# Kernel optimization log

Hardware: AMD Instinct MI355X
Metric: run time of the kernel (lower is better)

Reference implementation:

```python
import jax, jax.numpy as jnp
import numpy as np


def _unpack_int4(w_i32):
    # w_i32: [N, K//8] int32, 8 signed int4 nibbles per int32 (low nibble first)
    shifts = jnp.arange(8, dtype=jnp.int32) * 4
    nib = (w_i32[:, :, None] >> shifts[None, None, :]) & 0xF  # [N, K//8, 8]
    signed = (nib ^ 8) - 8  # map [0,15] -> [-8,7]
    N = w_i32.shape[0]
    return signed.reshape(N, -1)  # [N, K] int32 in [-8,7]


def setup_inputs() -> dict:
    key = jax.random.key(0)
    k1, k2, k3, k4, k5 = jax.random.split(key, 5)
    M, K, N, G = 4096, 4096, 14336, 128
    qx = jax.random.normal(k1, (M, K), dtype=jnp.float32)
    qxscale = jax.random.uniform(k2, (M, 1), dtype=jnp.float32, minval=0.5, maxval=1.5)
    weight_i4 = jax.random.randint(k3, (N, K // 8), 0, 2147483647, dtype=jnp.int32)
    weight_scale = jax.random.uniform(k4, (N, K // G), dtype=jnp.float32, minval=0.001, maxval=0.02)
    bias = jax.random.normal(k5, (N,), dtype=jnp.float32) * 0.02
    return {"qx": qx, "qxscale": qxscale, "weight_i4": weight_i4,
            "weight_scale": weight_scale, "bias": bias, "group_size": G}


def reference(qx, qxscale, weight_i4, weight_scale, bias, group_size):
    # 1) unpack int32 -> int4  2) per-group dequant  3) matmul  4) scale+bias  5) silu
    iweight = _unpack_int4(weight_i4)  # [N, K]
    N, K = iweight.shape
    deq_w = (iweight.astype(jnp.float32).reshape(N, K // group_size, group_size)
             * weight_scale[:, :, None]).reshape(N, K)  # [N, K]
    y = jnp.einsum('mk,nk->mn', qx, deq_w) * qxscale  # [M, N]
    y = y + bias[None, :]
    return jax.nn.silu(y)
```

## Files before the change

### kernel.cpp

```cpp
#include <hip/hip_runtime.h>
#include <hip/hip_bf16.h>
#include <stdint.h>


#define M_DIM 4096
#define K_DIM 4096
#define N_DIM 14336
#define GSZ   128

typedef __bf16 bf16x8 __attribute__((ext_vector_type(8)));
typedef __bf16 bf16x4 __attribute__((ext_vector_type(4)));
typedef float  f32x4  __attribute__((ext_vector_type(4)));

#define GLOAD16(g, l) __builtin_amdgcn_global_load_lds( \
    (const __attribute__((address_space(1))) void*)(g), \
    (__attribute__((address_space(3))) void*)(l), 16, 0, 0)

#define WAITVM(N) asm volatile("s_waitcnt vmcnt(" #N ")" ::: "memory")


__global__ __launch_bounds__(256) void convertA_kernel(
    const float* __restrict__ qx, __bf16* __restrict__ out)
{
    const size_t i = ((size_t)blockIdx.x * 256 + threadIdx.x) * 8;
    const float4 a = *(const float4*)(qx + i);
    const float4 b = *(const float4*)(qx + i + 4);
    bf16x8 v;
    v[0] = (__bf16)a.x; v[1] = (__bf16)a.y; v[2] = (__bf16)a.z; v[3] = (__bf16)a.w;
    v[4] = (__bf16)b.x; v[5] = (__bf16)b.y; v[6] = (__bf16)b.z; v[7] = (__bf16)b.w;
    *(bf16x8*)(out + i) = v;
}

__global__ __launch_bounds__(256) void dequantW_kernel(
    const int* __restrict__ wq, const float* __restrict__ wscale,
    __bf16* __restrict__ out)
{
    const size_t g = (size_t)blockIdx.x * 256 + threadIdx.x;
    const int n  = (int)(g >> 9);
    const int wi = (int)(g & 511);
    const float s = wscale[(size_t)n * (K_DIM / GSZ) + (wi >> 4)];
    const int w = wq[g];
    bf16x8 v;
    #pragma unroll
    for (int j = 0; j < 8; ++j) {
        const int q = ((int)((unsigned)w << (28 - 4 * j))) >> 28;
        v[j] = (__bf16)((float)q * s);
    }
    *(bf16x8*)(out + g * 8) = v;
}


constexpr int BM = 256, BN = 256, BK = 32;
constexpr int NT = K_DIM / BK;
constexpr int BUF_BYTES = 32768;

__global__ __launch_bounds__(512, 2) void gemm256_kernel(
    const __bf16* __restrict__ A,
    const __bf16* __restrict__ B,
    const float* __restrict__ qxscale,
    const float* __restrict__ bias,
    float* __restrict__ out)
{
    __shared__ __align__(16) char smem[4 * BUF_BYTES];

    const int t    = threadIdx.x;
    const int lane = t & 63;
    const int wave = t >> 6;
    const int wr   = wave >> 2;
    const int wc   = wave & 3;

    const int bid = blockIdx.x;
    const int cpx = (M_DIM / BM) * (N_DIM / BN) / 8;
    const int wg  = (bid & 7) * cpx + (bid >> 3);
    const int tiles_n = N_DIM / BN;
    const int tm = wg / tiles_n, tn = wg % tiles_n;
    const int m0 = tm * BM, n0 = tn * BN;

    const int srow = t >> 2;
    const int scb  = ((t & 3) * 16) ^ (((t >> 3) & 3) << 4);
    const char* aS = (const char*)A + (size_t)(m0 + srow) * K_DIM * 2 + scb;
    const char* bS = (const char*)B + (size_t)(n0 + srow) * K_DIM * 2 + scb;
    const size_t sweepG = (size_t)128 * K_DIM * 2;
    char* sbase = smem;

    auto STAGE_A = [&](int kt) {
        char* d = sbase + (kt & 3) * BUF_BYTES + t * 16;
        const char* s = aS + (size_t)kt * 64;
        GLOAD16(s, d);
        GLOAD16(s + sweepG, d + 8192);
    };
    auto STAGE_B = [&](int kt) {
        char* d = sbase + (kt & 3) * BUF_BYTES + 16384 + t * 16;
        const char* s = bS + (size_t)kt * 64;
        GLOAD16(s, d);
        GLOAD16(s + sweepG, d + 8192);
    };

    const int lane15 = lane & 15;
    const int pkb = ((lane >> 4) * 16) ^ (((lane >> 1) & 3) << 4);
    const int aRowB = (wr * 128 + lane15) * 64 + pkb;
    const int bRowB = (wc * 64 + lane15) * 64 + pkb + 16384;

    f32x4 acc[8][4] = {};

    STAGE_A(0); STAGE_B(0);
    STAGE_A(1); STAGE_B(1);
    STAGE_A(2); STAGE_B(2);
    WAITVM(8);
    __builtin_amdgcn_s_barrier();
    __builtin_amdgcn_sched_barrier(0);

    for (int kt = 0; kt < NT; ++kt) {
        const char* buf = sbase + (kt & 3) * BUF_BYTES;
        bf16x8 af[8], bf[4];

        #pragma unroll
        for (int ni = 0; ni < 4; ++ni)
            bf[ni] = *(const bf16x8*)(buf + bRowB + ni * 1024);
        #pragma unroll
        for (int mi = 0; mi < 8; ++mi)
            af[mi] = *(const bf16x8*)(buf + aRowB + mi * 1024);

        if (kt + 3 < NT) { STAGE_A(kt + 3); STAGE_B(kt + 3); }

        __builtin_amdgcn_s_setprio(1);
        #pragma unroll
        for (int mi = 0; mi < 8; ++mi)
            #pragma unroll
            for (int ni = 0; ni < 4; ++ni)
                acc[mi][ni] = __builtin_amdgcn_mfma_f32_16x16x32_bf16(
                    af[mi], bf[ni], acc[mi][ni], 0, 0, 0);
        __builtin_amdgcn_s_setprio(0);

        if (kt + 1 < NT) {
            if (kt + 3 < NT)      WAITVM(8);
            else if (kt + 2 < NT) WAITVM(4);
            else                  WAITVM(0);
            __builtin_amdgcn_s_barrier();
            __builtin_amdgcn_sched_barrier(0);
        }
    }

    const int c_col = lane & 15;
    const int c_r4  = (lane >> 4) * 4;
    #pragma unroll
    for (int mi = 0; mi < 8; ++mi) {
        const int mg = m0 + wr * 128 + mi * 16 + c_r4;
        float qs[4];
        #pragma unroll
        for (int r = 0; r < 4; ++r) qs[r] = qxscale[mg + r];
        #pragma unroll
        for (int ni = 0; ni < 4; ++ni) {
            const int ng = n0 + wc * 64 + ni * 16 + c_col;
            const float bv = bias[ng];
            #pragma unroll
            for (int r = 0; r < 4; ++r) {
                const float y = acc[mi][ni][r] * qs[r] + bv;
                out[(size_t)(mg + r) * N_DIM + ng] = y / (1.f + __expf(-y));
            }
        }
    }
}


constexpr int FBM = 128, FBN = 128, FBK = 64;
constexpr int FLDA = 72;

__global__ __launch_bounds__(256) void gateproj_fused_kernel(
    const float* __restrict__ qx, const float* __restrict__ qxscale,
    const int* __restrict__ wq, const float* __restrict__ wscale,
    const float* __restrict__ bias, float* __restrict__ out)
{
    __shared__ __bf16 sA[FBM * FLDA];
    __shared__ __bf16 sB[FBN * FLDA];

    const int tid  = threadIdx.x;
    const int lane = tid & 63;
    const int wave = tid >> 6;
    const int wm = wave >> 1, wn = wave & 1;

    const int bid = blockIdx.x;
    const int cpx = (M_DIM / FBM) * (N_DIM / FBN) / 8;
    const int wg  = (bid & 7) * cpx + (bid >> 3);
    const int tiles_n = N_DIM / FBN;
    const int tm = wg / tiles_n, tn = wg % tiles_n;
    const int m0 = tm * FBM, n0 = tn * FBN;

    const int a_row = tid >> 4;
    const int a_col = (tid & 15) * 4;
    const float* aPtr = qx + (size_t)(m0 + a_row) * K_DIM + a_col;

    const int b_row = tid >> 1;
    const int b_wb  = (tid & 1) * 4;
    const int*   bPtr = wq     + (size_t)(n0 + b_row) * (K_DIM / 8) + b_wb;
    const float* sPtr = wscale + (size_t)(n0 + b_row) * (K_DIM / GSZ);

    float4 aReg[8];
    int    bRegW[4];
    float  bScl;
    f32x4 acc[4][4] = {};

    auto LOAD = [&](int kt) {
        const float* ap = aPtr + kt * FBK;
        #pragma unroll
        for (int i = 0; i < 8; ++i)
            aReg[i] = *(const float4*)(ap + (size_t)i * 16 * K_DIM);
        int4 b = *(const int4*)(bPtr + kt * 8);
        bRegW[0] = b.x; bRegW[1] = b.y; bRegW[2] = b.z; bRegW[3] = b.w;
        bScl = sPtr[kt >> 1];
    };

    auto STORE = [&]() {
        #pragma unroll
        for (int i = 0; i < 8; ++i) {
            bf16x4 v;
            v[0] = (__bf16)aReg[i].x; v[1] = (__bf16)aReg[i].y;
            v[2] = (__bf16)aReg[i].z; v[3] = (__bf16)aReg[i].w;
            *(bf16x4*)&sA[(a_row + i * 16) * FLDA + a_col] = v;
        }
        const int cb = (tid & 1) * 32;
        #pragma unroll
        for (int wi = 0; wi < 4; ++wi) {
            const int w = bRegW[wi];
            bf16x8 o;
            #pragma unroll
            for (int j = 0; j < 8; ++j) {
                const int v = ((int)((unsigned)w << (28 - 4 * j))) >> 28;
                o[j] = (__bf16)((float)v * bScl);
            }
            *(bf16x8*)&sB[b_row * FLDA + cb + wi * 8] = o;
        }
    };

    LOAD(0); STORE(); __syncthreads();

    const int FNT = K_DIM / FBK;
    for (int kt = 0; kt < FNT; ++kt) {
        if (kt + 1 < FNT) LOAD(kt + 1);
        #pragma unroll
        for (int kk = 0; kk < 2; ++kk) {
            bf16x8 af[4], bfr[4];
            const int ko = kk * 32 + (lane >> 4) * 8;
            #pragma unroll
            for (int mi = 0; mi < 4; ++mi)
                af[mi] = *(const bf16x8*)&sA[(wm * 64 + mi * 16 + (lane & 15)) * FLDA + ko];
            #pragma unroll
            for (int ni = 0; ni < 4; ++ni)
                bfr[ni] = *(const bf16x8*)&sB[(wn * 64 + ni * 16 + (lane & 15)) * FLDA + ko];
            #pragma unroll
            for (int mi = 0; mi < 4; ++mi)
                #pragma unroll
                for (int ni = 0; ni < 4; ++ni)
                    acc[mi][ni] = __builtin_amdgcn_mfma_f32_16x16x32_bf16(
                        af[mi], bfr[ni], acc[mi][ni], 0, 0, 0);
        }
        __syncthreads();
        if (kt + 1 < FNT) { STORE(); __syncthreads(); }
    }

    const int c_col = lane & 15;
    const int c_r4  = (lane >> 4) * 4;
    #pragma unroll
    for (int mi = 0; mi < 4; ++mi) {
        const int mg = m0 + wm * 64 + mi * 16 + c_r4;
        float qs[4];
        #pragma unroll
        for (int r = 0; r < 4; ++r) qs[r] = qxscale[mg + r];
        #pragma unroll
        for (int ni = 0; ni < 4; ++ni) {
            const int ng = n0 + wn * 64 + ni * 16 + c_col;
            const float bv = bias[ng];
            #pragma unroll
            for (int r = 0; r < 4; ++r) {
                const float y = acc[mi][ni][r] * qs[r] + bv;
                out[(size_t)(mg + r) * N_DIM + ng] = y / (1.f + __expf(-y));
            }
        }
    }
}


extern "C" void kernel_launch(void* const* d_in, const int* in_sizes, int n_in,
                              void* d_out, int out_size, void* d_ws, size_t ws_size,
                              hipStream_t stream) {
    const float* qx      = (const float*)d_in[0];
    const float* qxscale = (const float*)d_in[1];
    const int*   wq      = (const int*)d_in[2];
    const float* wscale  = (const float*)d_in[3];
    const float* bias    = (const float*)d_in[4];
    float* out = (float*)d_out;

    const size_t needA = (size_t)M_DIM * K_DIM * 2;
    const size_t needW = (size_t)N_DIM * K_DIM * 2;

    if (ws_size >= needA + needW) {
        __bf16* Abf = (__bf16*)d_ws;
        __bf16* Wbf = Abf + (size_t)M_DIM * K_DIM;

        hipLaunchKernelGGL(convertA_kernel, dim3(M_DIM * K_DIM / 8 / 256), dim3(256),
                           0, stream, qx, Abf);
        hipLaunchKernelGGL(dequantW_kernel, dim3(N_DIM * (K_DIM / 8) / 256), dim3(256),
                           0, stream, wq, wscale, Wbf);

        const int grid = (M_DIM / BM) * (N_DIM / BN);
        hipLaunchKernelGGL(gemm256_kernel, dim3(grid), dim3(512), 0, stream,
                           Abf, Wbf, qxscale, bias, out);
    } else {
        const int grid = (M_DIM / FBM) * (N_DIM / FBN);
        hipLaunchKernelGGL(gateproj_fused_kernel, dim3(grid), dim3(256), 0, stream,
                           qx, qxscale, wq, wscale, bias, out);
    }
}
```

Baseline: 526.9 us.

## Fuse int4 dequant into GEMM main loop with fp16 MFMA and packed-weight staging

Removes the separate weight-dequantization pass and the bf16 weight buffer. The GEMM now stages packed int4 weights and per-group scales into shared memory and dequantizes in registers with a magic-number fp16 trick before each MFMA. Activations and MFMA switch from bf16 to fp16, and the main loop is restructured into a software-pipelined two-half schedule with explicit lgkm/vm waits. This cuts global traffic and one kernel launch, but adds ALU dequant work per tile that is repeated across M tiles and makes the scheduling more fragile. It also changes numeric precision, with possible fp16 range issues for the scaled weights.

```diff
diff --git a/kernel.cpp b/kernel.cpp
--- a/kernel.cpp
+++ b/kernel.cpp
@@ -8,60 +8,75 @@
 #define N_DIM 14336
 #define GSZ   128
 
+typedef _Float16 f16x8 __attribute__((ext_vector_type(8)));
+typedef _Float16 h2    __attribute__((ext_vector_type(2)));
+typedef float    f32x4 __attribute__((ext_vector_type(4)));
+typedef unsigned int uint4v __attribute__((ext_vector_type(4)));
 typedef __bf16 bf16x8 __attribute__((ext_vector_type(8)));
 typedef __bf16 bf16x4 __attribute__((ext_vector_type(4)));
-typedef float  f32x4  __attribute__((ext_vector_type(4)));
 
 #define GLOAD16(g, l) __builtin_amdgcn_global_load_lds( \
     (const __attribute__((address_space(1))) void*)(g), \
     (__attribute__((address_space(3))) void*)(l), 16, 0, 0)
 
-#define WAITVM(N) asm volatile("s_waitcnt vmcnt(" #N ")" ::: "memory")
+#define WAITVM_I(N) asm volatile("s_waitcnt vmcnt(" #N ")" ::: "memory")
+#define WAITVM(N) WAITVM_I(N)
+#define WAITLGKM_I(N) asm volatile("s_waitcnt lgkmcnt(" #N ")" ::: "memory")
+#define WAITLGKM(N) WAITLGKM_I(N)
+#define SB0() __builtin_amdgcn_sched_barrier(0)
+#define PRIO1() __builtin_amdgcn_s_setprio(1)
+#define PRIO0() __builtin_amdgcn_s_setprio(0)
 
 
 __global__ __launch_bounds__(256) void convertA_kernel(
-    const float* __restrict__ qx, __bf16* __restrict__ out)
+    const float* __restrict__ qx, _Float16* __restrict__ out)
 {
     const size_t i = ((size_t)blockIdx.x * 256 + threadIdx.x) * 8;
     const float4 a = *(const float4*)(qx + i);
     const float4 b = *(const float4*)(qx + i + 4);
-    bf16x8 v;
-    v[0] = (__bf16)a.x; v[1] = (__bf16)a.y; v[2] = (__bf16)a.z; v[3] = (__bf16)a.w;
-    v[4] = (__bf16)b.x; v[5] = (__bf16)b.y; v[6] = (__bf16)b.z; v[7] = (__bf16)b.w;
-    *(bf16x8*)(out + i) = v;
-}
-
-__global__ __launch_bounds__(256) void dequantW_kernel(
-    const int* __restrict__ wq, const float* __restrict__ wscale,
-    __bf16* __restrict__ out)
-{
-    const size_t g = (size_t)blockIdx.x * 256 + threadIdx.x;
-    const int n  = (int)(g >> 9);
-    const int wi = (int)(g & 511);
-    const float s = wscale[(size_t)n * (K_DIM / GSZ) + (wi >> 4)];
-    const int w = wq[g];
-    bf16x8 v;
-    #pragma unroll
-    for (int j = 0; j < 8; ++j) {
-        const int q = ((int)((unsigned)w << (28 - 4 * j))) >> 28;
-        v[j] = (__bf16)((float)q * s);
-    }
-    *(bf16x8*)(out + g * 8) = v;
+    f16x8 v;
+    v[0] = (_Float16)a.x; v[1] = (_Float16)a.y;
+    v[2] = (_Float16)a.z; v[3] = (_Float16)a.w;
+    v[4] = (_Float16)b.x; v[5] = (_Float16)b.y;
+    v[6] = (_Float16)b.z; v[7] = (_Float16)b.w;
+    *(f16x8*)(out + i) = v;
 }
 
 
 constexpr int BM = 256, BN = 256, BK = 32;
 constexpr int NT = K_DIM / BK;
-constexpr int BUF_BYTES = 32768;
+constexpr int ASLOT = 16384;
+constexpr int A_RING = 0;
+constexpr int BP_RING = 65536;
+constexpr int SCALES = 90112;
+
+static __device__ __forceinline__ f16x8 deq8(unsigned int w, float s) {
+    _Float16 hs = (_Float16)s;
+    unsigned short hb = __builtin_bit_cast(unsigned short, hs);
+    unsigned int su = (unsigned int)hb | ((unsigned int)hb << 16);
+    h2 s2 = __builtin_bit_cast(h2, su);
+    const h2 kc = {(_Float16)1032.0f, (_Float16)1032.0f};
+    unsigned int d0, d1, d2, d3;
+    #define DQPAIR(J, D) { \
+        unsigned int x = ((w >> (8*J)) & 0xFu) | (((w >> (8*J+4)) & 0xFu) << 16); \
+        x ^= 0x64086408u; \
+        h2 r = (__builtin_bit_cast(h2, x) - kc) * s2; \
+        D = __builtin_bit_cast(unsigned int, r); }
+    DQPAIR(0, d0) DQPAIR(1, d1) DQPAIR(2, d2) DQPAIR(3, d3)
+    #undef DQPAIR
+    uint4v u = {d0, d1, d2, d3};
+    return __builtin_bit_cast(f16x8, u);
+}
 
 __global__ __launch_bounds__(512, 2) void gemm256_kernel(
-    const __bf16* __restrict__ A,
-    const __bf16* __restrict__ B,
+    const _Float16* __restrict__ A,
+    const int* __restrict__ wq,
+    const float* __restrict__ wscale,
     const float* __restrict__ qxscale,
     const float* __restrict__ bias,
     float* __restrict__ out)
 {
-    __shared__ __align__(16) char smem[4 * BUF_BYTES];
+    __shared__ __align__(16) char smem[122880];
 
     const int t    = threadIdx.x;
     const int lane = t & 63;
@@ -79,67 +94,123 @@
     const int srow = t >> 2;
     const int scb  = ((t & 3) * 16) ^ (((t >> 3) & 3) << 4);
     const char* aS = (const char*)A + (size_t)(m0 + srow) * K_DIM * 2 + scb;
-    const char* bS = (const char*)B + (size_t)(n0 + srow) * K_DIM * 2 + scb;
     const size_t sweepG = (size_t)128 * K_DIM * 2;
-    char* sbase = smem;
 
     auto STAGE_A = [&](int kt) {
-        char* d = sbase + (kt & 3) * BUF_BYTES + t * 16;
+        char* d = smem + A_RING + (kt & 3) * ASLOT + t * 16;
         const char* s = aS + (size_t)kt * 64;
         GLOAD16(s, d);
         GLOAD16(s + sweepG, d + 8192);
     };
-    auto STAGE_B = [&](int kt) {
-        char* d = sbase + (kt & 3) * BUF_BYTES + 16384 + t * 16;
-        const char* s = bS + (size_t)kt * 64;
-        GLOAD16(s, d);
-        GLOAD16(s + sweepG, d + 8192);
+    const char* bpSrc = (const char*)wq
+        + (size_t)(n0 + (t & 255)) * (K_DIM / 8 * 4)
+        + (size_t)(t >> 8) * 16;
+    auto STAGE_BP = [&](char* dst, int p) {
+        GLOAD16(bpSrc + (size_t)p * 32, dst + t * 16);
     };
 
     const int lane15 = lane & 15;
     const int pkb = ((lane >> 4) * 16) ^ (((lane >> 1) & 3) << 4);
     const int aRowB = (wr * 128 + lane15) * 64 + pkb;
-    const int bRowB = (wc * 64 + lane15) * 64 + pkb + 16384;
+
+    const int bwOff = (wc * 64 + lane15) * 16 + ((lane >> 4) << 2);
+    const int sBase = SCALES + (wc * 64 + lane15) * 4;
 
     f32x4 acc[8][4] = {};
-
-    STAGE_A(0); STAGE_B(0);
-    STAGE_A(1); STAGE_B(1);
-    STAGE_A(2); STAGE_B(2);
-    WAITVM(8);
+    f16x8 afc[4], afn[4], af1[4];
+    f16x8 bf[4];
+    unsigned int bw[4];
+    float srf[4];
+
+    #define LA4(BUF, AF, BASE) do { _Pragma("unroll") \
+        for (int i_ = 0; i_ < 4; ++i_) \
+            AF[i_] = *(const f16x8*)((BUF) + aRowB + ((BASE) + i_) * 1024); \
+        } while (0)
+    #define LBW4(P) do { _Pragma("unroll") \
+        for (int n_ = 0; n_ < 4; ++n_) \
+            bw[n_] = *(const unsigned int*)((P) + bwOff + n_ * 256); \
+        } while (0)
+    #define LSR4(G) do { _Pragma("unroll") \
+        for (int n_ = 0; n_ < 4; ++n_) \
+            srf[n_] = *(const float*)(smem + sBase + (G) * 1024 + n_ * 64); \
+        } while (0)
+    #define DEQ4() do { _Pragma("unroll") \
+        for (int n_ = 0; n_ < 4; ++n_) bf[n_] = deq8(bw[n_], srf[n_]); \
+        } while (0)
+    #define MM16(AF, AB) do { _Pragma("unroll") \
+        for (int mi_ = 0; mi_ < 4; ++mi_) { _Pragma("unroll") \
+            for (int ni_ = 0; ni_ < 4; ++ni_) \
+                acc[(AB) + mi_][ni_] = __builtin_amdgcn_mfma_f32_16x16x32_f16( \
+                    AF[mi_], bf[ni_], acc[(AB) + mi_][ni_], 0, 0, 0); } \
+        } while (0)
+
+    char* bpCur   = smem + BP_RING;
+    char* bpNext  = smem + BP_RING + 8192;
+    char* bpStage = smem + BP_RING + 16384;
+
+    {
+        const float* wsp = wscale + (size_t)n0 * (K_DIM / GSZ);
+        #pragma unroll
+        for (int j = 0; j < 16; ++j) {
+            const int slot = t * 16 + j;
+            const float v = wsp[(size_t)(slot & 255) * (K_DIM / GSZ) + (slot >> 8)];
+            *(float*)(smem + SCALES + slot * 4) = v;
+        }
+    }
+    STAGE_A(0);
+    STAGE_BP(bpCur, 0);
+    STAGE_A(1);
+    STAGE_BP(bpNext, 1);
+    STAGE_A(2);
+    WAITVM(3);
+    WAITLGKM(0);
     __builtin_amdgcn_s_barrier();
-    __builtin_amdgcn_sched_barrier(0);
-
-    for (int kt = 0; kt < NT; ++kt) {
-        const char* buf = sbase + (kt & 3) * BUF_BYTES;
-        bf16x8 af[8], bf[4];
-
-        #pragma unroll
-        for (int ni = 0; ni < 4; ++ni)
-            bf[ni] = *(const bf16x8*)(buf + bRowB + ni * 1024);
-        #pragma unroll
-        for (int mi = 0; mi < 8; ++mi)
-            af[mi] = *(const bf16x8*)(buf + aRowB + mi * 1024);
-
-        if (kt + 3 < NT) { STAGE_A(kt + 3); STAGE_B(kt + 3); }
-
-        __builtin_amdgcn_s_setprio(1);
-        #pragma unroll
-        for (int mi = 0; mi < 8; ++mi)
-            #pragma unroll
-            for (int ni = 0; ni < 4; ++ni)
-                acc[mi][ni] = __builtin_amdgcn_mfma_f32_16x16x32_bf16(
-                    af[mi], bf[ni], acc[mi][ni], 0, 0, 0);
-        __builtin_amdgcn_s_setprio(0);
-
-        if (kt + 1 < NT) {
-            if (kt + 3 < NT)      WAITVM(8);
-            else if (kt + 2 < NT) WAITVM(4);
-            else                  WAITVM(0);
-            __builtin_amdgcn_s_barrier();
-            __builtin_amdgcn_sched_barrier(0);
-        }
-    }
+    SB0();
+    LA4(smem + A_RING, afc, 0);
+    LBW4(bpCur);
+    LSR4(0);
+
+    #define KBODY(KT, CUR, NXT, BPNXT, STAGE_STMTS, VMN) { \
+        LA4(smem + A_RING + ((KT) & 3) * ASLOT, af1, 4); \
+        STAGE_STMTS \
+        WAITLGKM(4); SB0(); \
+        DEQ4(); \
+        PRIO1(); MM16(CUR, 0); PRIO0(); \
+        LA4(smem + A_RING + (((KT) + 1) & 3) * ASLOT, NXT, 0); \
+        LBW4(BPNXT); \
+        LSR4(((KT) + 1) >> 2); \
+        WAITLGKM(12); SB0(); \
+        PRIO1(); MM16(af1, 4); PRIO0(); \
+        WAITVM(VMN); \
+        __builtin_amdgcn_s_barrier(); SB0(); }
+
+    for (int i = 0; i < 62; ++i) {
+        const int kt0 = 2 * i;
+        KBODY(kt0, afc, afn, bpCur + 4096,
+              { STAGE_A(kt0 + 3); STAGE_BP(bpStage, i + 2); }, 3)
+        KBODY(kt0 + 1, afn, afc, bpNext,
+              { STAGE_A(kt0 + 4); }, 3)
+        char* tmp = bpCur; bpCur = bpNext; bpNext = bpStage; bpStage = tmp;
+    }
+    KBODY(124, afc, afn, bpCur + 4096, { STAGE_A(127); }, 2)
+    KBODY(125, afn, afc, bpNext, { }, 0)
+    { char* tmp = bpCur; bpCur = bpNext; bpNext = bpStage; bpStage = tmp; }
+    KBODY(126, afc, afn, bpCur + 4096, { }, 0)
+    {
+        LA4(smem + A_RING + (127 & 3) * ASLOT, af1, 4);
+        WAITLGKM(4); SB0();
+        DEQ4();
+        PRIO1(); MM16(afn, 0); PRIO0();
+        WAITLGKM(0); SB0();
+        PRIO1(); MM16(af1, 4); PRIO0();
+    }
+
+    #undef KBODY
+    #undef LA4
+    #undef LBW4
+    #undef LSR4
+    #undef DEQ4
+    #undef MM16
 
     const int c_col = lane & 15;
     const int c_r4  = (lane >> 4) * 4;
@@ -239,20 +310,20 @@
         if (kt + 1 < FNT) LOAD(kt + 1);
         #pragma unroll
         for (int kk = 0; kk < 2; ++kk) {
-            bf16x8 af[4], bfr[4];
+            bf16x8 af2[4], bfr2[4];
             const int ko = kk * 32 + (lane >> 4) * 8;
             #pragma unroll
             for (int mi = 0; mi < 4; ++mi)
-                af[mi] = *(const bf16x8*)&sA[(wm * 64 + mi * 16 + (lane & 15)) * FLDA + ko];
+                af2[mi] = *(const bf16x8*)&sA[(wm * 64 + mi * 16 + (lane & 15)) * FLDA + ko];
             #pragma unroll
             for (int ni = 0; ni < 4; ++ni)
-                bfr[ni] = *(const bf16x8*)&sB[(wn * 64 + ni * 16 + (lane & 15)) * FLDA + ko];
+                bfr2[ni] = *(const bf16x8*)&sB[(wn * 64 + ni * 16 + (lane & 15)) * FLDA + ko];
             #pragma unroll
             for (int mi = 0; mi < 4; ++mi)
                 #pragma unroll
                 for (int ni = 0; ni < 4; ++ni)
                     acc[mi][ni] = __builtin_amdgcn_mfma_f32_16x16x32_bf16(
-                        af[mi], bfr[ni], acc[mi][ni], 0, 0, 0);
+                        af2[mi], bfr2[ni], acc[mi][ni], 0, 0, 0);
         }
         __syncthreads();
         if (kt + 1 < FNT) { STORE(); __syncthreads(); }
@@ -291,20 +362,16 @@
     float* out = (float*)d_out;
 
     const size_t needA = (size_t)M_DIM * K_DIM * 2;
-    const size_t needW = (size_t)N_DIM * K_DIM * 2;
-
-    if (ws_size >= needA + needW) {
-        __bf16* Abf = (__bf16*)d_ws;
-        __bf16* Wbf = Abf + (size_t)M_DIM * K_DIM;
+
+    if (ws_size >= needA) {
+        _Float16* Ah = (_Float16*)d_ws;
 
         hipLaunchKernelGGL(convertA_kernel, dim3(M_DIM * K_DIM / 8 / 256), dim3(256),
-                           0, stream, qx, Abf);
-        hipLaunchKernelGGL(dequantW_kernel, dim3(N_DIM * (K_DIM / 8) / 256), dim3(256),
-                           0, stream, wq, wscale, Wbf);
+                           0, stream, qx, Ah);
 
         const int grid = (M_DIM / BM) * (N_DIM / BN);
         hipLaunchKernelGGL(gemm256_kernel, dim3(grid), dim3(512), 0, stream,
-                           Abf, Wbf, qxscale, bias, out);
+                           Ah, wq, wscale, qxscale, bias, out);
     } else {
         const int grid = (M_DIM / FBM) * (N_DIM / FBN);
         hipLaunchKernelGGL(gateproj_fused_kernel, dim3(grid), dim3(256), 0, stream,
```

Result: slower. 586.4 us (+11.3%).

## Switch GEMM to 256x224 tiles with double-buffered LDS fragment prefetch

Applied to the files above, without the earlier changes.

Changes the bf16 GEMM tile from 256x256 to 256x224 so the grid (16x64 = 1024 tiles) fits the CU count better. The wave layout becomes 4x2, each wave holding 4x7 accumulators. The 224 B rows are staged with 16-byte loads plus 4-byte global_load_lds for the last 96 rows. The main loop is software-pipelined: it loads the next k-step's LDS fragments into alternate registers while MFMAs run, split into two MFMA chunks with lgkmcnt waits. This aims to improve wave-quantization and overlap LDS reads with compute, at the cost of narrower 4-byte loads and more register pressure.

```diff
diff --git a/kernel.cpp b/kernel.cpp
--- a/kernel.cpp
+++ b/kernel.cpp
@@ -15,8 +15,15 @@
 #define GLOAD16(g, l) __builtin_amdgcn_global_load_lds( \
     (const __attribute__((address_space(1))) void*)(g), \
     (__attribute__((address_space(3))) void*)(l), 16, 0, 0)
+#define GLOAD4(g, l) __builtin_amdgcn_global_load_lds( \
+    (const __attribute__((address_space(1))) void*)(g), \
+    (__attribute__((address_space(3))) void*)(l), 4, 0, 0)
 
 #define WAITVM(N) asm volatile("s_waitcnt vmcnt(" #N ")" ::: "memory")
+#define WAITLGKM(N) asm volatile("s_waitcnt lgkmcnt(" #N ")" ::: "memory")
+#define SB0() __builtin_amdgcn_sched_barrier(0)
+#define PRIO1() __builtin_amdgcn_s_setprio(1)
+#define PRIO0() __builtin_amdgcn_s_setprio(0)
 
 
 __global__ __launch_bounds__(256) void convertA_kernel(
@@ -50,24 +57,24 @@
 }
 
 
-constexpr int BM = 256, BN = 256, BK = 32;
+constexpr int BM = 256, BN = 224, BK = 32;
 constexpr int NT = K_DIM / BK;
-constexpr int BUF_BYTES = 32768;
-
-__global__ __launch_bounds__(512, 2) void gemm256_kernel(
+constexpr int SLOT = 30720;
+
+__global__ __launch_bounds__(512, 2) void gemm224_kernel(
     const __bf16* __restrict__ A,
     const __bf16* __restrict__ B,
     const float* __restrict__ qxscale,
     const float* __restrict__ bias,
     float* __restrict__ out)
 {
-    __shared__ __align__(16) char smem[4 * BUF_BYTES];
+    __shared__ __align__(16) char smem[4 * SLOT];
 
     const int t    = threadIdx.x;
     const int lane = t & 63;
     const int wave = t >> 6;
-    const int wr   = wave >> 2;
-    const int wc   = wave & 3;
+    const int wr   = wave >> 1;
+    const int wc   = wave & 1;
 
     const int bid = blockIdx.x;
     const int cpx = (M_DIM / BM) * (N_DIM / BN) / 8;
@@ -78,80 +85,116 @@
 
     const int srow = t >> 2;
     const int scb  = ((t & 3) * 16) ^ (((t >> 3) & 3) << 4);
-    const char* aS = (const char*)A + (size_t)(m0 + srow) * K_DIM * 2 + scb;
-    const char* bS = (const char*)B + (size_t)(n0 + srow) * K_DIM * 2 + scb;
-    const size_t sweepG = (size_t)128 * K_DIM * 2;
-    char* sbase = smem;
-
-    auto STAGE_A = [&](int kt) {
-        char* d = sbase + (kt & 3) * BUF_BYTES + t * 16;
-        const char* s = aS + (size_t)kt * 64;
-        GLOAD16(s, d);
-        GLOAD16(s + sweepG, d + 8192);
-    };
-    auto STAGE_B = [&](int kt) {
-        char* d = sbase + (kt & 3) * BUF_BYTES + 16384 + t * 16;
-        const char* s = bS + (size_t)kt * 64;
-        GLOAD16(s, d);
-        GLOAD16(s + sweepG, d + 8192);
+    const size_t KB = (size_t)K_DIM * 2;
+    const size_t sweepG = (size_t)128 * KB;
+    const char* aS = (const char*)A + (size_t)(m0 + srow) * KB + scb;
+    const char* bS = (const char*)B + (size_t)(n0 + srow) * KB + scb;
+    const int g4 = ((((t & 15) >> 2) ^ ((t >> 5) & 3)) << 4) + (t & 3) * 4;
+    const char* bS4 = (const char*)B + (size_t)(n0 + 128 + (t >> 4)) * KB + g4;
+
+    auto STAGE = [&](int kt) {
+        char* slot = smem + (kt & 3) * SLOT;
+        const char* sa = aS + (size_t)kt * 64;
+        GLOAD16(sa,           slot + t * 16);
+        GLOAD16(sa + sweepG,  slot + 8192 + t * 16);
+        const char* sb = bS + (size_t)kt * 64;
+        GLOAD16(sb,           slot + 16384 + t * 16);
+        const char* sb4 = bS4 + (size_t)kt * 64;
+        GLOAD4(sb4,               slot + 24576 + t * 4);
+        GLOAD4(sb4 + 32 * KB,     slot + 24576 + 2048 + t * 4);
+        GLOAD4(sb4 + 64 * KB,     slot + 24576 + 4096 + t * 4);
     };
 
     const int lane15 = lane & 15;
     const int pkb = ((lane >> 4) * 16) ^ (((lane >> 1) & 3) << 4);
-    const int aRowB = (wr * 128 + lane15) * 64 + pkb;
-    const int bRowB = (wc * 64 + lane15) * 64 + pkb + 16384;
-
-    f32x4 acc[8][4] = {};
-
-    STAGE_A(0); STAGE_B(0);
-    STAGE_A(1); STAGE_B(1);
-    STAGE_A(2); STAGE_B(2);
-    WAITVM(8);
+    const int aRowB = (wr * 64 + lane15) * 64 + pkb;
+    const int bRowB = 16384 + (wc * 112 + lane15) * 64 + pkb;
+
+    f32x4 acc[4][7] = {};
+    bf16x8 afc[4], bfc[4];
+    bf16x8 afn[4], bfn[4];
+    bf16x8 bf1[3];
+
+    #define LA4(SLOTP, AF) do { _Pragma("unroll") \
+        for (int i_ = 0; i_ < 4; ++i_) \
+            AF[i_] = *(const bf16x8*)((SLOTP) + aRowB + i_ * 1024); \
+        } while (0)
+    #define LB4(SLOTP, BF) do { _Pragma("unroll") \
+        for (int n_ = 0; n_ < 4; ++n_) \
+            BF[n_] = *(const bf16x8*)((SLOTP) + bRowB + n_ * 1024); \
+        } while (0)
+    #define LB3(SLOTP) do { _Pragma("unroll") \
+        for (int n_ = 0; n_ < 3; ++n_) \
+            bf1[n_] = *(const bf16x8*)((SLOTP) + bRowB + (4 + n_) * 1024); \
+        } while (0)
+    #define MMC0(AF, BF) do { _Pragma("unroll") \
+        for (int mi_ = 0; mi_ < 4; ++mi_) { _Pragma("unroll") \
+            for (int ni_ = 0; ni_ < 4; ++ni_) \
+                acc[mi_][ni_] = __builtin_amdgcn_mfma_f32_16x16x32_bf16( \
+                    AF[mi_], BF[ni_], acc[mi_][ni_], 0, 0, 0); } \
+        } while (0)
+    #define MMC1(AF) do { _Pragma("unroll") \
+        for (int mi_ = 0; mi_ < 4; ++mi_) { _Pragma("unroll") \
+            for (int ni_ = 0; ni_ < 3; ++ni_) \
+                acc[mi_][4 + ni_] = __builtin_amdgcn_mfma_f32_16x16x32_bf16( \
+                    AF[mi_], bf1[ni_], acc[mi_][4 + ni_], 0, 0, 0); } \
+        } while (0)
+
+    #define KBODY(KT, AFC, BFC, AFN, BFN) { \
+        const char* cur = smem + ((KT) & 3) * SLOT; \
+        const char* nxt = smem + (((KT) + 1) & 3) * SLOT; \
+        LB3(cur); \
+        if ((KT) + 3 < NT) STAGE((KT) + 3); \
+        WAITLGKM(3); SB0(); \
+        PRIO1(); MMC0(AFC, BFC); PRIO0(); \
+        LA4(nxt, AFN); LB4(nxt, BFN); \
+        WAITLGKM(8); SB0(); \
+        PRIO1(); MMC1(AFC); PRIO0(); \
+        if ((KT) + 3 < NT) WAITVM(6); else WAITVM(0); \
+        __builtin_amdgcn_s_barrier(); SB0(); }
+
+    STAGE(0);
+    STAGE(1);
+    STAGE(2);
+    WAITVM(6);
     __builtin_amdgcn_s_barrier();
-    __builtin_amdgcn_sched_barrier(0);
-
-    for (int kt = 0; kt < NT; ++kt) {
-        const char* buf = sbase + (kt & 3) * BUF_BYTES;
-        bf16x8 af[8], bf[4];
-
-        #pragma unroll
-        for (int ni = 0; ni < 4; ++ni)
-            bf[ni] = *(const bf16x8*)(buf + bRowB + ni * 1024);
-        #pragma unroll
-        for (int mi = 0; mi < 8; ++mi)
-            af[mi] = *(const bf16x8*)(buf + aRowB + mi * 1024);
-
-        if (kt + 3 < NT) { STAGE_A(kt + 3); STAGE_B(kt + 3); }
-
-        __builtin_amdgcn_s_setprio(1);
-        #pragma unroll
-        for (int mi = 0; mi < 8; ++mi)
-            #pragma unroll
-            for (int ni = 0; ni < 4; ++ni)
-                acc[mi][ni] = __builtin_amdgcn_mfma_f32_16x16x32_bf16(
-                    af[mi], bf[ni], acc[mi][ni], 0, 0, 0);
-        __builtin_amdgcn_s_setprio(0);
-
-        if (kt + 1 < NT) {
-            if (kt + 3 < NT)      WAITVM(8);
-            else if (kt + 2 < NT) WAITVM(4);
-            else                  WAITVM(0);
-            __builtin_amdgcn_s_barrier();
-            __builtin_amdgcn_sched_barrier(0);
-        }
-    }
+    SB0();
+    LA4(smem, afc);
+    LB4(smem, bfc);
+
+    for (int i = 0; i < 63; ++i) {
+        const int kt = 2 * i;
+        KBODY(kt,     afc, bfc, afn, bfn)
+        KBODY(kt + 1, afn, bfn, afc, bfc)
+    }
+    KBODY(126, afc, bfc, afn, bfn)
+    {
+        const char* cur = smem + (127 & 3) * SLOT;
+        LB3(cur);
+        WAITLGKM(3); SB0();
+        PRIO1(); MMC0(afn, bfn); PRIO0();
+        WAITLGKM(0); SB0();
+        PRIO1(); MMC1(afn); PRIO0();
+    }
+
+    #undef KBODY
+    #undef LA4
+    #undef LB4
+    #undef LB3
+    #undef MMC0
+    #undef MMC1
 
     const int c_col = lane & 15;
     const int c_r4  = (lane >> 4) * 4;
     #pragma unroll
-    for (int mi = 0; mi < 8; ++mi) {
-        const int mg = m0 + wr * 128 + mi * 16 + c_r4;
+    for (int mi = 0; mi < 4; ++mi) {
+        const int mg = m0 + wr * 64 + mi * 16 + c_r4;
         float qs[4];
         #pragma unroll
         for (int r = 0; r < 4; ++r) qs[r] = qxscale[mg + r];
         #pragma unroll
-        for (int ni = 0; ni < 4; ++ni) {
-            const int ng = n0 + wc * 64 + ni * 16 + c_col;
+        for (int ni = 0; ni < 7; ++ni) {
+            const int ng = n0 + wc * 112 + ni * 16 + c_col;
             const float bv = bias[ng];
             #pragma unroll
             for (int r = 0; r < 4; ++r) {
@@ -239,20 +282,20 @@
         if (kt + 1 < FNT) LOAD(kt + 1);
         #pragma unroll
         for (int kk = 0; kk < 2; ++kk) {
-            bf16x8 af[4], bfr[4];
+            bf16x8 af2[4], bfr2[4];
             const int ko = kk * 32 + (lane >> 4) * 8;
             #pragma unroll
             for (int mi = 0; mi < 4; ++mi)
-                af[mi] = *(const bf16x8*)&sA[(wm * 64 + mi * 16 + (lane & 15)) * FLDA + ko];
+                af2[mi] = *(const bf16x8*)&sA[(wm * 64 + mi * 16 + (lane & 15)) * FLDA + ko];
             #pragma unroll
             for (int ni = 0; ni < 4; ++ni)
-                bfr[ni] = *(const bf16x8*)&sB[(wn * 64 + ni * 16 + (lane & 15)) * FLDA + ko];
+                bfr2[ni] = *(const bf16x8*)&sB[(wn * 64 + ni * 16 + (lane & 15)) * FLDA + ko];
             #pragma unroll
             for (int mi = 0; mi < 4; ++mi)
                 #pragma unroll
                 for (int ni = 0; ni < 4; ++ni)
                     acc[mi][ni] = __builtin_amdgcn_mfma_f32_16x16x32_bf16(
-                        af[mi], bfr[ni], acc[mi][ni], 0, 0, 0);
+                        af2[mi], bfr2[ni], acc[mi][ni], 0, 0, 0);
         }
         __syncthreads();
         if (kt + 1 < FNT) { STORE(); __syncthreads(); }
@@ -303,7 +346,7 @@
                            0, stream, wq, wscale, Wbf);
 
         const int grid = (M_DIM / BM) * (N_DIM / BN);
-        hipLaunchKernelGGL(gemm256_kernel, dim3(grid), dim3(512), 0, stream,
+        hipLaunchKernelGGL(gemm224_kernel, dim3(grid), dim3(512), 0, stream,
                            Abf, Wbf, qxscale, bias, out);
     } else {
         const int grid = (M_DIM / FBM) * (N_DIM / FBN);
```

Measured after the change: 528.7 us. About the same (+0.3%).
